# Kernel optimization log

Measured on AMD Instinct MI355X. Metric: run time of the kernel, lower is better.

The kernel has to match this reference:

```python
import jax, jax.numpy as jnp
import numpy as np

B, S, HID = 2, 2048, 2560
NH, NKV, HD = 8, 4, 256
Q_SIZE, KV_SIZE = NH * HD, NKV * HD
SCALE = 256.0 ** -0.5
SLIDING_WINDOW = 1024 - 1  # config.sliding_window - 1
ROPE_BASE = 10000.0
EPS = 1e-6


def rmsnorm(x, w, eps=EPS):
    xf = x.astype(jnp.float32)
    out = xf * jax.lax.rsqrt(jnp.mean(xf * xf, axis=-1, keepdims=True) + eps)
    return (out * (1.0 + w.astype(jnp.float32))).astype(x.dtype)


def apply_rope(x, positions):
    # x: [B,S,H,D], neox style (rotate halves)
    d = x.shape[-1]
    inv_freq = 1.0 / (ROPE_BASE ** (jnp.arange(0, d, 2, dtype=jnp.float32) / d))
    freqs = positions.astype(jnp.float32)[..., None] * inv_freq  # [B,S,d/2]
    cos = jnp.cos(freqs)[:, :, None, :]
    sin = jnp.sin(freqs)[:, :, None, :]
    x1, x2 = x[..., : d // 2], x[..., d // 2:]
    return jnp.concatenate([x1 * cos - x2 * sin, x2 * cos + x1 * sin], axis=-1).astype(x.dtype)


def setup_inputs() -> dict:
    key = jax.random.key(0)
    ks = jax.random.split(key, 4)
    positions = jnp.broadcast_to(jnp.arange(S, dtype=jnp.int32)[None, :], (B, S))
    hidden_states = jax.random.normal(ks[0], (B, S, HID), dtype=jnp.float32)
    attention_mask = jnp.ones((B, S), dtype=jnp.int32)
    Wqkv = jax.random.normal(ks[1], (HID, Q_SIZE + 2 * KV_SIZE), dtype=jnp.float32) * (HID ** -0.5)
    Wo = jax.random.normal(ks[2], (Q_SIZE, HID), dtype=jnp.float32) * (Q_SIZE ** -0.5)
    q_norm_w = jnp.zeros((HD,), dtype=jnp.float32)
    k_norm_w = jnp.zeros((HD,), dtype=jnp.float32)
    return {"positions": positions, "hidden_states": hidden_states,
            "attention_mask": attention_mask, "Wqkv": Wqkv, "Wo": Wo,
            "q_norm_w": q_norm_w, "k_norm_w": k_norm_w}


def reference(positions, hidden_states, attention_mask, Wqkv, Wo, q_norm_w, k_norm_w):
    b, s, _ = hidden_states.shape
    qkv = hidden_states @ Wqkv
    q, k, v = jnp.split(qkv, [Q_SIZE, Q_SIZE + KV_SIZE], axis=-1)
    q = q.reshape(b, s, NH, HD)
    k = k.reshape(b, s, NKV, HD)
    v = v.reshape(b, s, NKV, HD)
    q = rmsnorm(q, q_norm_w)
    k = rmsnorm(k, k_norm_w)
    q = apply_rope(q, positions)
    k = apply_rope(k, positions)

    # additive mask, replicating source exactly
    idx = jnp.arange(s)
    causal = idx[None, :] > idx[:, None]             # triu(diag=1)
    too_far = (idx[None, :] - idx[:, None]) > SLIDING_WINDOW
    base_mask = causal | too_far                      # [S,S]
    key_pad = attention_mask.astype(bool) == False    # [B,S]
    masked = base_mask[None, None, :, :] | key_pad[:, None, None, :]  # [B,1,S,S]
    add_mask = jnp.where(masked, -jnp.inf, 0.0).astype(jnp.float32)

    # GQA: group queries over kv heads
    g = NH // NKV
    qg = q.reshape(b, s, NKV, g, HD)
    scores = jnp.einsum('bsmgd,btmd->bmgst', qg, k) * SCALE  # [B,NKV,g,S,S]
    scores = scores + add_mask[:, :, None, :, :]
    probs = jax.nn.softmax(scores, axis=-1)
    out = jnp.einsum('bmgst,btmd->bsmgd', probs, v)           # [B,S,NKV,g,HD]
    out = out.reshape(b, s, NH * HD)
    return out @ Wo
```

## Files before the change

kernel.cpp:

```cpp
#include <hip/hip_runtime.h>
#include <stdint.h>

#define S_LEN 2048
#define BATCH 2
#define HIDDEN 2560
#define NH 8
#define NKV 4
#define HD 256
#define QSZ (NH*HD)
#define NQKV 4096
#define MROWS (BATCH*S_LEN)
#define SCALE_ATT 0.0625f

using bf16x8 = __attribute__((__ext_vector_type__(8))) __bf16;
using f32x4  = __attribute__((__ext_vector_type__(4))) float;
using s16x8  = __attribute__((__ext_vector_type__(8))) short;

union B8u { s16x8 s; bf16x8 b; };
union I4B8 { int4 i; bf16x8 b; };

__device__ __forceinline__ unsigned short f2bf(float x){
  unsigned u = __float_as_uint(x);
  u += 0x7fffu + ((u >> 16) & 1u);
  return (unsigned short)(u >> 16);
}
__device__ __forceinline__ bf16x8 ld_bf8(const unsigned short* p){
  B8u u; u.s = *reinterpret_cast<const s16x8*>(p); return u.b;
}
__device__ __forceinline__ f32x4 mfma16(bf16x8 a, bf16x8 b, f32x4 c){
  return __builtin_amdgcn_mfma_f32_16x16x32_bf16(a, b, c, 0, 0, 0);
}
__device__ __forceinline__ void gload16(const void* g, void* l){
  __builtin_amdgcn_global_load_lds((const __attribute__((address_space(1))) void*)g,
                                   (__attribute__((address_space(3))) void*)l,
                                   16, 0, 0);
}
__device__ __forceinline__ int cvtpk(float lo, float hi){
  int r;
  asm("v_cvt_pk_bf16_f32 %0, %1, %2" : "=v"(r) : "v"(lo), "v"(hi));
  return r;
}

__global__ __launch_bounds__(256) void cast_bf16_kernel(
    const float* __restrict__ in, unsigned short* __restrict__ out, int n)
{
  int i = (blockIdx.x * 256 + threadIdx.x) * 4;
  if (i < n){
    float4 v = *reinterpret_cast<const float4*>(in + i);
    ushort4 o;
    o.x = f2bf(v.x); o.y = f2bf(v.y); o.z = f2bf(v.z); o.w = f2bf(v.w);
    *reinterpret_cast<ushort4*>(out + i) = o;
  }
}

__global__ __launch_bounds__(256) void tcast_kernel(
    const float* __restrict__ in, unsigned short* __restrict__ out, int R, int C)
{
  __shared__ float t[32][33];
  int c0 = blockIdx.x * 32, r0 = blockIdx.y * 32;
  int tx = threadIdx.x & 31, ty = threadIdx.x >> 5;
#pragma unroll
  for (int ii = 0; ii < 4; ii++)
    t[ty + ii*8][tx] = in[(size_t)(r0 + ty + ii*8) * C + c0 + tx];
  __syncthreads();
#pragma unroll
  for (int ii = 0; ii < 4; ii++)
    out[(size_t)(c0 + ty + ii*8) * R + r0 + tx] = f2bf(t[tx][ty + ii*8]);
}

__global__ __launch_bounds__(256) void ropetab_kernel(
    const int* __restrict__ positions, float* __restrict__ ct, float* __restrict__ st)
{
  const int cix = blockIdx.x;
  const int b   = blockIdx.y;
  const float kln = -9.210340371976184f / 128.0f;
  const float inv = expf((float)cix * kln);
  float* cp = ct + ((size_t)b * 128 + cix) * 2048;
  float* sp = st + ((size_t)b * 128 + cix) * 2048;
  for (int s = threadIdx.x; s < S_LEN; s += 256){
    float fpos = (float)positions[b * S_LEN + s];
    float sv, cv;
    sincosf(fpos * inv, &sv, &cv);
    cp[s] = cv;
    sp[s] = sv;
  }
}

__global__ __launch_bounds__(512, 2) void gemm_qkv_kernel(
    const unsigned short* __restrict__ A,
    const unsigned short* __restrict__ BT,
    const float* __restrict__ qw, const float* __restrict__ kw,
    const float* __restrict__ ct, const float* __restrict__ st,
    unsigned short* __restrict__ qB,
    unsigned short* __restrict__ kB,
    unsigned short* __restrict__ vT)
{
  __shared__ unsigned short Ab[2][256 * 64];
  __shared__ unsigned short Bb[2][256 * 64];

  const int K = HIDDEN;
  const int nbn = 16;
  const int tid  = threadIdx.x;
  const int lane = tid & 63;
  const int wid  = tid >> 6;
  const int wm = wid >> 2, wn = wid & 3;
  const int lq = lane & 15, lk = lane >> 4;

  const int cpx = gridDim.x >> 3;
  const int wg  = (blockIdx.x & 7) * cpx + (blockIdx.x >> 3);
  const int bm = wg / nbn, bn = wg % nbn;

  const int l8 = lane >> 3;
  const int sl = ((lane & 7) ^ l8) * 8;
  const unsigned short* agS = A  + (size_t)(bm*256 + wid*16 + l8) * K + sl;
  const unsigned short* bgS = BT + (size_t)(bn*256 + wid*16 + l8) * K + sl;

  f32x4 acc[4][4][2] = {};
  bf16x8 a[4][2], b[2][2];

#define STA(c, h, tt) do {                                                    \
    unsigned short* d = &Ab[c][(h)*8192 + wid*1024];                          \
    const unsigned short* s = agS + (size_t)(h)*128*K + (size_t)(tt)*64;      \
    gload16(s, d); gload16(s + 8*(size_t)K, d + 512);                         \
  } while (0)
#define STB(c, h, tt) do {                                                    \
    unsigned short* d = &Bb[c][(h)*8192 + wid*1024];                          \
    const unsigned short* s = bgS + (size_t)(h)*128*K + (size_t)(tt)*64;      \
    gload16(s, d); gload16(s + 8*(size_t)K, d + 512);                         \
  } while (0)
#define LDA(qa) do {                                                          \
    _Pragma("unroll") for (int m = 0; m < 4; m++)                             \
    _Pragma("unroll") for (int kk = 0; kk < 2; kk++)                          \
      a[m][kk] = ld_bf8(&Ab[cur][((qa)*128 + wm*64 + m*16 + lq)*64            \
                                 + (((kk*4 + lk) ^ (lq & 7)) << 3)]);         \
  } while (0)
#define LDB(qb) do {                                                          \
    _Pragma("unroll") for (int n = 0; n < 2; n++)                             \
    _Pragma("unroll") for (int kk = 0; kk < 2; kk++)                          \
      b[n][kk] = ld_bf8(&Bb[cur][((qb)*128 + wn*32 + n*16 + lq)*64            \
                                 + (((kk*4 + lk) ^ (lq & 7)) << 3)]);         \
  } while (0)
#define MM(qi) do {                                                           \
    __builtin_amdgcn_s_setprio(1);                                            \
    _Pragma("unroll") for (int m = 0; m < 4; m++)                             \
    _Pragma("unroll") for (int n = 0; n < 2; n++)                             \
    _Pragma("unroll") for (int kk = 0; kk < 2; kk++)                          \
      acc[qi][m][n] = mfma16(a[m][kk], b[n][kk], acc[qi][m][n]);              \
    __builtin_amdgcn_s_setprio(0);                                            \
  } while (0)
#define BARR __builtin_amdgcn_s_barrier()
#define VM(n) asm volatile("s_waitcnt vmcnt(" #n ")" ::: "memory")

  STA(0, 0, 0); STB(0, 0, 0); STB(0, 1, 0); STA(0, 1, 0);
  VM(4); BARR;

  const int NT = K >> 6;
  for (int t = 0; t < NT - 1; ++t){
    const int cur = t & 1, nxt = cur ^ 1;
    LDA(0); LDB(0); STA(nxt, 0, t+1);
    BARR; MM(0); VM(4); BARR;
    LDB(1);         STB(nxt, 0, t+1);
    BARR; MM(1); VM(4); BARR;
    LDA(1);         STB(nxt, 1, t+1);
    BARR; MM(2);        BARR;
    LDB(0);         STA(nxt, 1, t+1);
    BARR; MM(3); VM(4); BARR;
  }
  {
    const int cur = (NT - 1) & 1;
    LDA(0); LDB(0); BARR; MM(0); VM(2); BARR;
    LDB(1);         BARR; MM(1); VM(0); BARR;
    LDA(1);         BARR; MM(2);        BARR;
    LDB(0);         BARR; MM(3);        BARR;
  }
#undef STA
#undef STB
#undef LDA
#undef LDB
#undef MM
#undef BARR
#undef VM

  __syncthreads();
  const int b_  = bm >> 3;
  const int sb0 = (bm & 7) * 256;

  if (bn >= 12){
    const int mhv = bn - 12;
#pragma unroll
    for (int qi = 0; qi < 4; qi++){
      const int qa = qi >> 1, qb = (qi ^ (qi >> 1)) & 1;
#pragma unroll
      for (int m = 0; m < 4; m++){
        const int s0 = sb0 + qa*128 + wm*64 + m*16 + lk*4;
#pragma unroll
        for (int n = 0; n < 2; n++){
          const int d = qb*128 + wn*32 + n*16 + lq;
          ushort4 o;
          o.x = f2bf(acc[qi][m][n][0]);
          o.y = f2bf(acc[qi][m][n][1]);
          o.z = f2bf(acc[qi][m][n][2]);
          o.w = f2bf(acc[qi][m][n][3]);
          *reinterpret_cast<ushort4*>(
              vT + ((size_t)((b_*NKV + mhv)*HD + d))*S_LEN + s0) = o;
        }
      }
    }
  } else {
    float* red = (float*)Ab;
    float part[2][4][4];
#pragma unroll
    for (int qa = 0; qa < 2; qa++){
      const int qiA = qa ? 3 : 0, qiB = qa ? 2 : 1;
#pragma unroll
      for (int m = 0; m < 4; m++)
#pragma unroll
      for (int i = 0; i < 4; i++){
        float s = 0.f;
#pragma unroll
        for (int n = 0; n < 2; n++)
          s += acc[qiA][m][n][i]*acc[qiA][m][n][i]
             + acc[qiB][m][n][i]*acc[qiB][m][n][i];
        s += __shfl_xor(s, 1, 64);
        s += __shfl_xor(s, 2, 64);
        s += __shfl_xor(s, 4, 64);
        s += __shfl_xor(s, 8, 64);
        part[qa][m][i] = s;
      }
    }
    if (lq == 0){
#pragma unroll
      for (int qa = 0; qa < 2; qa++)
#pragma unroll
      for (int m = 0; m < 4; m++)
#pragma unroll
      for (int i = 0; i < 4; i++)
        red[wn*256 + qa*128 + wm*64 + m*16 + lk*4 + i] = part[qa][m][i];
    }
    __syncthreads();
    float rsv[2][4][4];
#pragma unroll
    for (int qa = 0; qa < 2; qa++)
#pragma unroll
    for (int m = 0; m < 4; m++)
#pragma unroll
    for (int i = 0; i < 4; i++){
      const int row = qa*128 + wm*64 + m*16 + lk*4 + i;
      float tt = red[row] + red[256 + row] + red[512 + row] + red[768 + row];
      rsv[qa][m][i] = rsqrtf(tt * (1.0f/256.0f) + 1e-6f);
    }
    const float* wv = (bn < 8) ? qw : kw;
    unsigned short* dstB = (bn < 8)
      ? qB + ((size_t)(b_*NH  + bn      ) * S_LEN) * HD
      : kB + ((size_t)(b_*NKV + (bn - 8)) * S_LEN) * HD;
    const float* ctb = ct + (size_t)b_ * 128 * 2048;
    const float* stb = st + (size_t)b_ * 128 * 2048;
#pragma unroll
    for (int qa = 0; qa < 2; qa++){
      const int qiA = qa ? 3 : 0, qiB = qa ? 2 : 1;
#pragma unroll
      for (int m = 0; m < 4; m++){
        const int s0 = sb0 + qa*128 + wm*64 + m*16 + lk*4;
#pragma unroll
        for (int n = 0; n < 2; n++){
          const int c0 = wn*32 + n*16 + lq;
          const float w0 = 1.0f + wv[c0];
          const float w1 = 1.0f + wv[c0 + 128];
          const float4 c4 = *reinterpret_cast<const float4*>(ctb + (size_t)c0*2048 + s0);
          const float4 s4 = *reinterpret_cast<const float4*>(stb + (size_t)c0*2048 + s0);
#pragma unroll
          for (int i = 0; i < 4; i++){
            const float rs_ = rsv[qa][m][i];
            const float y0 = acc[qiA][m][n][i] * rs_ * w0;
            const float y1 = acc[qiB][m][n][i] * rs_ * w1;
            const float cc = (&c4.x)[i], ss = (&s4.x)[i];
            unsigned short* p = dstB + (size_t)(s0 + i) * HD;
            p[c0]       = f2bf(y0 * cc - y1 * ss);
            p[c0 + 128] = f2bf(y1 * cc + y0 * ss);
          }
        }
      }
    }
  }
}

__global__ __launch_bounds__(512, 2) void gemm256_kernel(
    const unsigned short* __restrict__ A,
    const unsigned short* __restrict__ BT,
    float* __restrict__ C,
    int N, int K, int nbn)
{
  __shared__ unsigned short Ab[2][256 * 64];
  __shared__ unsigned short Bb[2][256 * 64];

  const int tid  = threadIdx.x;
  const int lane = tid & 63;
  const int wid  = tid >> 6;
  const int wm = wid >> 2, wn = wid & 3;
  const int lq = lane & 15, lk = lane >> 4;

  const int cpx = gridDim.x >> 3;
  const int wg  = (blockIdx.x & 7) * cpx + (blockIdx.x >> 3);
  const int bm = wg / nbn, bn = wg % nbn;

  const int l8 = lane >> 3;
  const int sl = ((lane & 7) ^ l8) * 8;
  const unsigned short* agS = A  + (size_t)(bm*256 + wid*16 + l8) * K + sl;
  const unsigned short* bgS = BT + (size_t)(bn*256 + wid*16 + l8) * K + sl;

  f32x4 acc[4][4][2] = {};
  bf16x8 a[4][2], b[2][2];

#define STA(c, h, tt) do {                                                    \
    unsigned short* d = &Ab[c][(h)*8192 + wid*1024];                          \
    const unsigned short* s = agS + (size_t)(h)*128*K + (size_t)(tt)*64;      \
    gload16(s, d); gload16(s + 8*(size_t)K, d + 512);                         \
  } while (0)
#define STB(c, h, tt) do {                                                    \
    unsigned short* d = &Bb[c][(h)*8192 + wid*1024];                          \
    const unsigned short* s = bgS + (size_t)(h)*128*K + (size_t)(tt)*64;      \
    gload16(s, d); gload16(s + 8*(size_t)K, d + 512);                         \
  } while (0)
#define LDA(qa) do {                                                          \
    _Pragma("unroll") for (int m = 0; m < 4; m++)                             \
    _Pragma("unroll") for (int kk = 0; kk < 2; kk++)                          \
      a[m][kk] = ld_bf8(&Ab[cur][((qa)*128 + wm*64 + m*16 + lq)*64            \
                                 + (((kk*4 + lk) ^ (lq & 7)) << 3)]);         \
  } while (0)
#define LDB(qb) do {                                                          \
    _Pragma("unroll") for (int n = 0; n < 2; n++)                             \
    _Pragma("unroll") for (int kk = 0; kk < 2; kk++)                          \
      b[n][kk] = ld_bf8(&Bb[cur][((qb)*128 + wn*32 + n*16 + lq)*64            \
                                 + (((kk*4 + lk) ^ (lq & 7)) << 3)]);         \
  } while (0)
#define MM(qi) do {                                                           \
    __builtin_amdgcn_s_setprio(1);                                            \
    _Pragma("unroll") for (int m = 0; m < 4; m++)                             \
    _Pragma("unroll") for (int n = 0; n < 2; n++)                             \
    _Pragma("unroll") for (int kk = 0; kk < 2; kk++)                          \
      acc[qi][m][n] = mfma16(a[m][kk], b[n][kk], acc[qi][m][n]);              \
    __builtin_amdgcn_s_setprio(0);                                            \
  } while (0)
#define BARR __builtin_amdgcn_s_barrier()
#define VM(n) asm volatile("s_waitcnt vmcnt(" #n ")" ::: "memory")

  STA(0, 0, 0); STB(0, 0, 0); STB(0, 1, 0); STA(0, 1, 0);
  VM(4); BARR;

  const int NT = K >> 6;
  for (int t = 0; t < NT - 1; ++t){
    const int cur = t & 1, nxt = cur ^ 1;
    LDA(0); LDB(0); STA(nxt, 0, t+1);
    BARR; MM(0); VM(4); BARR;
    LDB(1);         STB(nxt, 0, t+1);
    BARR; MM(1); VM(4); BARR;
    LDA(1);         STB(nxt, 1, t+1);
    BARR; MM(2);        BARR;
    LDB(0);         STA(nxt, 1, t+1);
    BARR; MM(3); VM(4); BARR;
  }
  {
    const int cur = (NT - 1) & 1;
    LDA(0); LDB(0); BARR; MM(0); VM(2); BARR;
    LDB(1);         BARR; MM(1); VM(0); BARR;
    LDA(1);         BARR; MM(2);        BARR;
    LDB(0);         BARR; MM(3);        BARR;
  }
#undef STA
#undef STB
#undef LDA
#undef LDB
#undef MM
#undef BARR
#undef VM

#pragma unroll
  for (int qi = 0; qi < 4; qi++){
    const int qa = qi >> 1;
    const int qb = (qi ^ (qi >> 1)) & 1;
    const int r0 = bm*256 + qa*128 + wm*64;
    const int c0 = bn*256 + qb*128 + wn*32;
#pragma unroll
    for (int m = 0; m < 4; m++)
#pragma unroll
      for (int n = 0; n < 2; n++)
#pragma unroll
        for (int i = 0; i < 4; i++)
          C[(size_t)(r0 + m*16 + lk*4 + i) * N + (c0 + n*16 + lq)] = acc[qi][m][n][i];
  }
}

__global__ void maskbits_kernel(const int* __restrict__ amask, unsigned* __restrict__ bm,
                                int* __restrict__ ctr)
{
  int t = threadIdx.x;
  int b = t >> 6, tile = t & 63;
  unsigned m = 0;
  for (int j = 0; j < 32; j++)
    m |= (amask[b * S_LEN + tile * 32 + j] != 0 ? 1u : 0u) << j;
  bm[t] = m;
  if (t < 8) ctr[t] = 0;
}

__global__ __launch_bounds__(256) void attn_kernel(
    const unsigned short* __restrict__ qB,
    const unsigned short* __restrict__ kB,
    const unsigned short* __restrict__ vT,
    const unsigned* __restrict__ bmG,
    unsigned short* __restrict__ attnO,
    int* __restrict__ ctr)
{
  __shared__ unsigned short Kb[4][32 * 256];
  __shared__ unsigned short Vb[4][256 * 32];
  __shared__ unsigned bm_lds[64];
  __shared__ int s_idx;

  const int tid  = threadIdx.x;
  const int lane = tid & 63, wid = tid >> 6;
  const int c  = blockIdx.x & 7;
  const int mh = c & 3, b = c >> 2;
  const int h  = mh * 2 + (wid >> 1);
  const int lq = lane & 15, lk = lane >> 4;

  if (tid < 64) bm_lds[tid] = bmG[(b << 6) + tid];

  const unsigned short* kbase = kB + (size_t)(b * NKV + mh) * S_LEN * HD;
  const unsigned short* vbase = vT + (size_t)(b * NKV + mh) * HD * S_LEN;
  const int krow0 = wid * 2 + (lane >> 5);
  const int kgsrc = (lane & 31) ^ (krow0 & 7);
  const unsigned short* kg0 = kbase + (size_t)krow0 * HD + kgsrc * 8;
  const int vd0 = wid * 16 + (lane >> 2);
  const int vgsrc = (lane & 3) ^ ((lane >> 3) & 3);
  const unsigned short* vg0 = vbase + (size_t)vd0 * S_LEN + vgsrc * 8;

#define STAGE_K(buf, ktv)                                                      \
  do {                                                                         \
    _Pragma("unroll")                                                          \
    for (int r = 0; r < 4; r++)                                                \
      gload16(kg0 + (size_t)(ktv) * HD + r * (8 * HD),                         \
              &Kb[buf][wid * 512 + r * 2048]);                                 \
  } while (0)
#define STAGE_V(buf, ktv)                                                      \
  do {                                                                         \
    _Pragma("unroll")                                                          \
    for (int r = 0; r < 4; r++)                                                \
      gload16(vg0 + (ktv) + (size_t)r * (64 * S_LEN),                          \
              &Vb[buf][wid * 512 + r * 2048]);                                 \
  } while (0)

  for (;;){
    if (tid == 0) s_idx = atomicAdd(&ctr[c], 1);
    __syncthreads();
    const int idx = s_idx;
    __syncthreads();
    if (idx >= 64) break;
    const int qt = 63 - idx;

    const int q0 = qt * 32 + (wid & 1) * 16;
    const int q  = q0 + lq;

    const unsigned short* qbase = qB + ((size_t)(b * NH + h) * S_LEN + q0 + lq) * HD + lk * 8;
    bf16x8 aq[8];
#pragma unroll
    for (int ks = 0; ks < 8; ks++) aq[ks] = ld_bf8(qbase + ks * 32);
    asm volatile("s_waitcnt vmcnt(0)" ::: "memory");

    float mi = -__builtin_inff(), li = 0.f;
    f32x4 oacc[16] = {};

    STAGE_K(0, 0); STAGE_V(0, 0);
    if (qt >= 1){ STAGE_K(1, 32); STAGE_V(1, 32); }
    if (qt >= 2){ STAGE_K(2, 64); STAGE_V(2, 64); }
    if (qt >= 3){ STAGE_K(3, 96); STAGE_V(3, 96); }

    const int npairs = (qt >> 1) + 1;
    for (int p = 0; p < npairs; ++p){
      const int ktA = p * 64;
      const int ktB = ktA + 32;
      const bool hasB = (2*p + 1 <= qt);
      const int bufA = (2*p) & 3, bufB = (2*p + 1) & 3;

      const int ahead = qt - 2*p - 1;
      if (ahead >= 2)      asm volatile("s_waitcnt vmcnt(16)" ::: "memory");
      else if (ahead == 1) asm volatile("s_waitcnt vmcnt(8)"  ::: "memory");
      else                 asm volatile("s_waitcnt vmcnt(0)"  ::: "memory");
      __syncthreads();

      f32x4 sA0 = {0.f,0.f,0.f,0.f}, sA1 = {0.f,0.f,0.f,0.f};
      f32x4 sB0 = {0.f,0.f,0.f,0.f}, sB1 = {0.f,0.f,0.f,0.f};
      if (hasB){
#pragma unroll
        for (int ks = 0; ks < 8; ks++){
          const int slot = (((ks * 4 + lk) ^ (lq & 7)) << 3);
          bf16x8 kA0 = ld_bf8(&Kb[bufA][lq * 256 + slot]);
          bf16x8 kA1 = ld_bf8(&Kb[bufA][(16 + lq) * 256 + slot]);
          bf16x8 kB0 = ld_bf8(&Kb[bufB][lq * 256 + slot]);
          bf16x8 kB1 = ld_bf8(&Kb[bufB][(16 + lq) * 256 + slot]);
          sA0 = mfma16(kA0, aq[ks], sA0);
          sA1 = mfma16(kA1, aq[ks], sA1);
          sB0 = mfma16(kB0, aq[ks], sB0);
          sB1 = mfma16(kB1, aq[ks], sB1);
        }
      } else {
#pragma unroll
        for (int ks = 0; ks < 8; ks++){
          const int slot = (((ks * 4 + lk) ^ (lq & 7)) << 3);
          bf16x8 kA0 = ld_bf8(&Kb[bufA][lq * 256 + slot]);
          bf16x8 kA1 = ld_bf8(&Kb[bufA][(16 + lq) * 256 + slot]);
          sA0 = mfma16(kA0, aq[ks], sA0);
          sA1 = mfma16(kA1, aq[ks], sA1);
        }
      }

      const unsigned mA = bm_lds[ktA >> 5];
      const unsigned mB = bm_lds[(ktB >> 5) & 63];
      const int koff = lk * 4;
      float vA0[4], vA1[4], vB0[4], vB1[4];
#pragma unroll
      for (int j2 = 0; j2 < 4; j2++){
        const bool a0 = (ktA + koff + j2 <= q)      && ((mA >> (koff + j2)) & 1u);
        const bool a1 = (ktA + 16 + koff + j2 <= q) && ((mA >> (16 + koff + j2)) & 1u);
        vA0[j2] = a0 ? sA0[j2] * SCALE_ATT : -__builtin_inff();
        vA1[j2] = a1 ? sA1[j2] * SCALE_ATT : -__builtin_inff();
      }
      if (hasB){
#pragma unroll
        for (int j2 = 0; j2 < 4; j2++){
          const bool b0 = (ktB + koff + j2 <= q)      && ((mB >> (koff + j2)) & 1u);
          const bool b1 = (ktB + 16 + koff + j2 <= q) && ((mB >> (16 + koff + j2)) & 1u);
          vB0[j2] = b0 ? sB0[j2] * SCALE_ATT : -__builtin_inff();
          vB1[j2] = b1 ? sB1[j2] * SCALE_ATT : -__builtin_inff();
        }
      } else {
#pragma unroll
        for (int j2 = 0; j2 < 4; j2++){ vB0[j2] = -__builtin_inff(); vB1[j2] = -__builtin_inff(); }
      }
      float tm = fmaxf(fmaxf(fmaxf(vA0[0], vA0[1]), fmaxf(vA0[2], vA0[3])),
                       fmaxf(fmaxf(vA1[0], vA1[1]), fmaxf(vA1[2], vA1[3])));
      if (hasB){
        float tb = fmaxf(fmaxf(fmaxf(vB0[0], vB0[1]), fmaxf(vB0[2], vB0[3])),
                         fmaxf(fmaxf(vB1[0], vB1[1]), fmaxf(vB1[2], vB1[3])));
        tm = fmaxf(tm, tb);
      }
      tm = fmaxf(tm, __shfl_xor(tm, 16, 64));
      tm = fmaxf(tm, __shfl_xor(tm, 32, 64));

      float pA0[4], pA1[4], pB0[4], pB1[4];
      if (__all(tm <= mi + 8.0f)){
        const float mns = fmaxf(mi, -1e30f);
#pragma unroll
        for (int j2 = 0; j2 < 4; j2++){
          pA0[j2] = __expf(vA0[j2] - mns); pA1[j2] = __expf(vA1[j2] - mns);
          pB0[j2] = __expf(vB0[j2] - mns); pB1[j2] = __expf(vB1[j2] - mns);
        }
        float rs = (pA0[0]+pA0[1])+(pA0[2]+pA0[3])+(pA1[0]+pA1[1])+(pA1[2]+pA1[3])
                 + (pB0[0]+pB0[1])+(pB0[2]+pB0[3])+(pB1[0]+pB1[1])+(pB1[2]+pB1[3]);
        rs += __shfl_xor(rs, 16, 64);
        rs += __shfl_xor(rs, 32, 64);
        li += rs;
      } else {
        const float mn  = fmaxf(mi, tm);
        const float mns = fmaxf(mn, -1e30f);
#pragma unroll
        for (int j2 = 0; j2 < 4; j2++){
          pA0[j2] = __expf(vA0[j2] - mns); pA1[j2] = __expf(vA1[j2] - mns);
          pB0[j2] = __expf(vB0[j2] - mns); pB1[j2] = __expf(vB1[j2] - mns);
        }
        const float a_ = __expf(mi - mns);
        float rs = (pA0[0]+pA0[1])+(pA0[2]+pA0[3])+(pA1[0]+pA1[1])+(pA1[2]+pA1[3])
                 + (pB0[0]+pB0[1])+(pB0[2]+pB0[3])+(pB1[0]+pB1[1])+(pB1[2]+pB1[3]);
        rs += __shfl_xor(rs, 16, 64);
        rs += __shfl_xor(rs, 32, 64);
        li = li * a_ + rs;
        mi = mn;
        float av[4];
#pragma unroll
        for (int i = 0; i < 4; i++)
          av[i] = __shfl(a_, (lane & 48) | (lk * 4 + i), 64);
#pragma unroll
        for (int db = 0; db < 16; db++){
          f32x4 o = oacc[db];
#pragma unroll
          for (int i = 0; i < 4; i++) o[i] *= av[i];
          oacc[db] = o;
        }
      }

      const int sA_ = (((lk & 1) * 2) << 4) | lq;
      const int sB_ = sA_ + 16;
      const bool hi = (lk >= 2);
      I4B8 pauA, pauB;
      {
        const int w0 = cvtpk(pA0[0], pA0[1]), w1 = cvtpk(pA0[2], pA0[3]);
        const int w2 = cvtpk(pA1[0], pA1[1]), w3 = cvtpk(pA1[2], pA1[3]);
        const int a0 = __shfl(w0, sA_, 64), a1 = __shfl(w1, sA_, 64);
        const int b0 = __shfl(w0, sB_, 64), b1 = __shfl(w1, sB_, 64);
        const int c0w = __shfl(w2, sA_, 64), c1w = __shfl(w3, sA_, 64);
        const int d0w = __shfl(w2, sB_, 64), d1w = __shfl(w3, sB_, 64);
        pauA.i.x = hi ? c0w : a0;
        pauA.i.y = hi ? c1w : a1;
        pauA.i.z = hi ? d0w : b0;
        pauA.i.w = hi ? d1w : b1;
      }
      if (hasB){
        const int w0 = cvtpk(pB0[0], pB0[1]), w1 = cvtpk(pB0[2], pB0[3]);
        const int w2 = cvtpk(pB1[0], pB1[1]), w3 = cvtpk(pB1[2], pB1[3]);
        const int a0 = __shfl(w0, sA_, 64), a1 = __shfl(w1, sA_, 64);
        const int b0 = __shfl(w0, sB_, 64), b1 = __shfl(w1, sB_, 64);
        const int c0w = __shfl(w2, sA_, 64), c1w = __shfl(w3, sA_, 64);
        const int d0w = __shfl(w2, sB_, 64), d1w = __shfl(w3, sB_, 64);
        pauB.i.x = hi ? c0w : a0;
        pauB.i.y = hi ? c1w : a1;
        pauB.i.z = hi ? d0w : b0;
        pauB.i.w = hi ? d1w : b1;
      }

      const int vslot = (lk ^ ((lq >> 1) & 3)) << 3;
      if (hasB){
#pragma unroll
        for (int db = 0; db < 16; db++){
          bf16x8 vfA = ld_bf8(&Vb[bufA][(db * 16 + lq) * 32 + vslot]);
          bf16x8 vfB = ld_bf8(&Vb[bufB][(db * 16 + lq) * 32 + vslot]);
          f32x4 o = mfma16(pauA.b, vfA, oacc[db]);
          oacc[db] = mfma16(pauB.b, vfB, o);
        }
      } else {
#pragma unroll
        for (int db = 0; db < 16; db++){
          bf16x8 vfA = ld_bf8(&Vb[bufA][(db * 16 + lq) * 32 + vslot]);
          oacc[db] = mfma16(pauA.b, vfA, oacc[db]);
        }
      }

      __syncthreads();
      if (2*p + 4 <= qt){ STAGE_K(bufA, ktA + 128); STAGE_V(bufA, ktA + 128); }
      if (2*p + 5 <= qt){ STAGE_K(bufB, ktB + 128); STAGE_V(bufB, ktB + 128); }
    }

#pragma unroll
    for (int i = 0; i < 4; i++){
      const float lf = __shfl(li, (lane & 48) | (lk * 4 + i), 64);
      const float inv = 1.0f / lf;
      unsigned short* orow = attnO + (size_t)(b * S_LEN + q0 + lk*4 + i) * QSZ + h * HD + lq;
#pragma unroll
      for (int db = 0; db < 16; db++)
        orow[db * 16] = f2bf(oacc[db][i] * inv);
    }
  }
#undef STAGE_K
#undef STAGE_V
}

extern "C" void kernel_launch(void* const* d_in, const int* in_sizes, int n_in,
                              void* d_out, int out_size, void* d_ws, size_t ws_size,
                              hipStream_t stream)
{
  const int*   positions = (const int*)  d_in[0];
  const float* hidden    = (const float*)d_in[1];
  const int*   amask     = (const int*)  d_in[2];
  const float* Wqkv      = (const float*)d_in[3];
  const float* Wo        = (const float*)d_in[4];
  const float* qw        = (const float*)d_in[5];
  const float* kw        = (const float*)d_in[6];
  float* out = (float*)d_out;

  char* ws = (char*)d_ws;
  unsigned short* hB    = (unsigned short*)(ws);
  unsigned short* attnO = (unsigned short*)(ws);
  unsigned short* WqT   = (unsigned short*)(ws + 20971520);
  unsigned short* WoT   = (unsigned short*)(ws + 41943040);
  float*          ct    = (float*)        (ws + 52428800);
  float*          st    = (float*)        (ws + 56623104);
  unsigned short* qb    = (unsigned short*)(ws + 119537664);
  unsigned short* kb    = (unsigned short*)(ws + 136314880);
  unsigned short* vt    = (unsigned short*)(ws + 144703488);
  unsigned*       bm    = (unsigned*)     (ws + 153092096);
  int*            ctr   = (int*)          (ws + 153092608);

  cast_bf16_kernel<<<dim3(MROWS * HIDDEN / 1024), 256, 0, stream>>>(hidden, hB, MROWS * HIDDEN);
  tcast_kernel<<<dim3(NQKV / 32, HIDDEN / 32), 256, 0, stream>>>(Wqkv, WqT, HIDDEN, NQKV);
  tcast_kernel<<<dim3(HIDDEN / 32, QSZ / 32), 256, 0, stream>>>(Wo, WoT, QSZ, HIDDEN);
  maskbits_kernel<<<dim3(1), 128, 0, stream>>>(amask, bm, ctr);
  ropetab_kernel<<<dim3(128, BATCH), 256, 0, stream>>>(positions, ct, st);

  gemm_qkv_kernel<<<dim3((MROWS/256) * (NQKV/256)), 512, 0, stream>>>(
      hB, WqT, qw, kw, ct, st, qb, kb, vt);

  attn_kernel<<<dim3(256), 256, 0, stream>>>(qb, kb, vt, bm, attnO, ctr);

  gemm256_kernel<<<dim3((MROWS/256) * (HIDDEN/256)), 512, 0, stream>>>(
      attnO, WoT, out, HIDDEN, QSZ, HIDDEN/256);
}
```

Before: 317.7 us.

## Process two 16-row query blocks per wave to reuse K/V fragments

Each wave now handles 32 query rows (two 16-row sub-tiles) per work item, so every K and V fragment read from LDS feeds two MFMAs. Work items drop from 64 to 32 per (batch, kv-head) group. The K/V staging goes from four buffers with paired tiles to two buffers with one tile per step. This halves LDS traffic per unit of compute and frees shared memory. In exchange it doubles the accumulator and Q registers, which may lower occupancy, and coarser query tiles add causal-masked waste and worse load balance near the diagonal.

```diff
diff --git a/kernel.cpp b/kernel.cpp
--- a/kernel.cpp
+++ b/kernel.cpp
@@ -410,8 +410,8 @@
     unsigned short* __restrict__ attnO,
     int* __restrict__ ctr)
 {
-  __shared__ unsigned short Kb[4][32 * 256];
-  __shared__ unsigned short Vb[4][256 * 32];
+  __shared__ unsigned short Kb[2][32 * 256];
+  __shared__ unsigned short Vb[2][256 * 32];
   __shared__ unsigned bm_lds[64];
   __shared__ int s_idx;
 
@@ -453,143 +453,131 @@
     __syncthreads();
     const int idx = s_idx;
     __syncthreads();
-    if (idx >= 64) break;
-    const int qt = 63 - idx;
-
-    const int q0 = qt * 32 + (wid & 1) * 16;
-    const int q  = q0 + lq;
-
-    const unsigned short* qbase = qB + ((size_t)(b * NH + h) * S_LEN + q0 + lq) * HD + lk * 8;
-    bf16x8 aq[8];
-#pragma unroll
-    for (int ks = 0; ks < 8; ks++) aq[ks] = ld_bf8(qbase + ks * 32);
+    if (idx >= 32) break;
+    const int qt = 31 - idx;
+
+    const int q0 = qt * 64 + (wid & 1) * 32;
+    const int qr0 = q0 + lq;
+    const int qr1 = q0 + 16 + lq;
+
+    const unsigned short* qbase = qB + ((size_t)(b * NH + h) * S_LEN + qr0) * HD + lk * 8;
+    bf16x8 aq0[8], aq1[8];
+#pragma unroll
+    for (int ks = 0; ks < 8; ks++){
+      aq0[ks] = ld_bf8(qbase + ks * 32);
+      aq1[ks] = ld_bf8(qbase + 16 * HD + ks * 32);
+    }
     asm volatile("s_waitcnt vmcnt(0)" ::: "memory");
 
-    float mi = -__builtin_inff(), li = 0.f;
-    f32x4 oacc[16] = {};
-
-    STAGE_K(0, 0); STAGE_V(0, 0);
-    if (qt >= 1){ STAGE_K(1, 32); STAGE_V(1, 32); }
-    if (qt >= 2){ STAGE_K(2, 64); STAGE_V(2, 64); }
-    if (qt >= 3){ STAGE_K(3, 96); STAGE_V(3, 96); }
-
-    const int npairs = (qt >> 1) + 1;
-    for (int p = 0; p < npairs; ++p){
-      const int ktA = p * 64;
-      const int ktB = ktA + 32;
-      const bool hasB = (2*p + 1 <= qt);
-      const int bufA = (2*p) & 3, bufB = (2*p + 1) & 3;
-
-      const int ahead = qt - 2*p - 1;
-      if (ahead >= 2)      asm volatile("s_waitcnt vmcnt(16)" ::: "memory");
-      else if (ahead == 1) asm volatile("s_waitcnt vmcnt(8)"  ::: "memory");
-      else                 asm volatile("s_waitcnt vmcnt(0)"  ::: "memory");
+    float mi0 = -__builtin_inff(), li0 = 0.f;
+    float mi1 = -__builtin_inff(), li1 = 0.f;
+    f32x4 oacc0[16] = {};
+    f32x4 oacc1[16] = {};
+
+    const int ktmax = qt * 64 + 32;
+
+    STAGE_K(0, 0);  STAGE_V(0, 0);
+    STAGE_K(1, 32); STAGE_V(1, 32);
+
+    int cur = 0;
+    for (int kt = 0; kt <= ktmax; kt += 32, cur ^= 1){
+      if (kt < ktmax) asm volatile("s_waitcnt vmcnt(8)" ::: "memory");
+      else            asm volatile("s_waitcnt vmcnt(0)" ::: "memory");
       __syncthreads();
 
       f32x4 sA0 = {0.f,0.f,0.f,0.f}, sA1 = {0.f,0.f,0.f,0.f};
-      f32x4 sB0 = {0.f,0.f,0.f,0.f}, sB1 = {0.f,0.f,0.f,0.f};
-      if (hasB){
-#pragma unroll
-        for (int ks = 0; ks < 8; ks++){
-          const int slot = (((ks * 4 + lk) ^ (lq & 7)) << 3);
-          bf16x8 kA0 = ld_bf8(&Kb[bufA][lq * 256 + slot]);
-          bf16x8 kA1 = ld_bf8(&Kb[bufA][(16 + lq) * 256 + slot]);
-          bf16x8 kB0 = ld_bf8(&Kb[bufB][lq * 256 + slot]);
-          bf16x8 kB1 = ld_bf8(&Kb[bufB][(16 + lq) * 256 + slot]);
-          sA0 = mfma16(kA0, aq[ks], sA0);
-          sA1 = mfma16(kA1, aq[ks], sA1);
-          sB0 = mfma16(kB0, aq[ks], sB0);
-          sB1 = mfma16(kB1, aq[ks], sB1);
+      f32x4 sC0 = {0.f,0.f,0.f,0.f}, sC1 = {0.f,0.f,0.f,0.f};
+#pragma unroll
+      for (int ks = 0; ks < 8; ks++){
+        const int slot = (((ks * 4 + lk) ^ (lq & 7)) << 3);
+        bf16x8 kf0 = ld_bf8(&Kb[cur][lq * 256 + slot]);
+        bf16x8 kf1 = ld_bf8(&Kb[cur][(16 + lq) * 256 + slot]);
+        sA0 = mfma16(kf0, aq0[ks], sA0);
+        sA1 = mfma16(kf1, aq0[ks], sA1);
+        sC0 = mfma16(kf0, aq1[ks], sC0);
+        sC1 = mfma16(kf1, aq1[ks], sC1);
+      }
+
+      const unsigned mask32 = bm_lds[kt >> 5];
+      const int koff = lk * 4;
+      float vA0[4], vA1[4], vC0[4], vC1[4];
+#pragma unroll
+      for (int j2 = 0; j2 < 4; j2++){
+        const bool m0 = ((mask32 >> (koff + j2)) & 1u);
+        const bool m1 = ((mask32 >> (16 + koff + j2)) & 1u);
+        const int k0 = kt + koff + j2, k1 = kt + 16 + koff + j2;
+        vA0[j2] = (k0 <= qr0 && m0) ? sA0[j2] * SCALE_ATT : -__builtin_inff();
+        vA1[j2] = (k1 <= qr0 && m1) ? sA1[j2] * SCALE_ATT : -__builtin_inff();
+        vC0[j2] = (k0 <= qr1 && m0) ? sC0[j2] * SCALE_ATT : -__builtin_inff();
+        vC1[j2] = (k1 <= qr1 && m1) ? sC1[j2] * SCALE_ATT : -__builtin_inff();
+      }
+      float tm0 = fmaxf(fmaxf(fmaxf(vA0[0], vA0[1]), fmaxf(vA0[2], vA0[3])),
+                        fmaxf(fmaxf(vA1[0], vA1[1]), fmaxf(vA1[2], vA1[3])));
+      float tm1 = fmaxf(fmaxf(fmaxf(vC0[0], vC0[1]), fmaxf(vC0[2], vC0[3])),
+                        fmaxf(fmaxf(vC1[0], vC1[1]), fmaxf(vC1[2], vC1[3])));
+      tm0 = fmaxf(tm0, __shfl_xor(tm0, 16, 64));
+      tm0 = fmaxf(tm0, __shfl_xor(tm0, 32, 64));
+      tm1 = fmaxf(tm1, __shfl_xor(tm1, 16, 64));
+      tm1 = fmaxf(tm1, __shfl_xor(tm1, 32, 64));
+
+      float pA0[4], pA1[4], pC0[4], pC1[4];
+      if (__all(tm0 <= mi0 + 8.0f && tm1 <= mi1 + 8.0f)){
+        const float mns0 = fmaxf(mi0, -1e30f);
+        const float mns1 = fmaxf(mi1, -1e30f);
+#pragma unroll
+        for (int j2 = 0; j2 < 4; j2++){
+          pA0[j2] = __expf(vA0[j2] - mns0); pA1[j2] = __expf(vA1[j2] - mns0);
+          pC0[j2] = __expf(vC0[j2] - mns1); pC1[j2] = __expf(vC1[j2] - mns1);
         }
+        float rs0 = (pA0[0]+pA0[1])+(pA0[2]+pA0[3])+(pA1[0]+pA1[1])+(pA1[2]+pA1[3]);
+        float rs1 = (pC0[0]+pC0[1])+(pC0[2]+pC0[3])+(pC1[0]+pC1[1])+(pC1[2]+pC1[3]);
+        rs0 += __shfl_xor(rs0, 16, 64);
+        rs0 += __shfl_xor(rs0, 32, 64);
+        rs1 += __shfl_xor(rs1, 16, 64);
+        rs1 += __shfl_xor(rs1, 32, 64);
+        li0 += rs0;
+        li1 += rs1;
       } else {
-#pragma unroll
-        for (int ks = 0; ks < 8; ks++){
-          const int slot = (((ks * 4 + lk) ^ (lq & 7)) << 3);
-          bf16x8 kA0 = ld_bf8(&Kb[bufA][lq * 256 + slot]);
-          bf16x8 kA1 = ld_bf8(&Kb[bufA][(16 + lq) * 256 + slot]);
-          sA0 = mfma16(kA0, aq[ks], sA0);
-          sA1 = mfma16(kA1, aq[ks], sA1);
+        const float mn0  = fmaxf(mi0, tm0);
+        const float mn1  = fmaxf(mi1, tm1);
+        const float mns0 = fmaxf(mn0, -1e30f);
+        const float mns1 = fmaxf(mn1, -1e30f);
+#pragma unroll
+        for (int j2 = 0; j2 < 4; j2++){
+          pA0[j2] = __expf(vA0[j2] - mns0); pA1[j2] = __expf(vA1[j2] - mns0);
+          pC0[j2] = __expf(vC0[j2] - mns1); pC1[j2] = __expf(vC1[j2] - mns1);
         }
-      }
-
-      const unsigned mA = bm_lds[ktA >> 5];
-      const unsigned mB = bm_lds[(ktB >> 5) & 63];
-      const int koff = lk * 4;
-      float vA0[4], vA1[4], vB0[4], vB1[4];
-#pragma unroll
-      for (int j2 = 0; j2 < 4; j2++){
-        const bool a0 = (ktA + koff + j2 <= q)      && ((mA >> (koff + j2)) & 1u);
-        const bool a1 = (ktA + 16 + koff + j2 <= q) && ((mA >> (16 + koff + j2)) & 1u);
-        vA0[j2] = a0 ? sA0[j2] * SCALE_ATT : -__builtin_inff();
-        vA1[j2] = a1 ? sA1[j2] * SCALE_ATT : -__builtin_inff();
-      }
-      if (hasB){
-#pragma unroll
-        for (int j2 = 0; j2 < 4; j2++){
-          const bool b0 = (ktB + koff + j2 <= q)      && ((mB >> (koff + j2)) & 1u);
-          const bool b1 = (ktB + 16 + koff + j2 <= q) && ((mB >> (16 + koff + j2)) & 1u);
-          vB0[j2] = b0 ? sB0[j2] * SCALE_ATT : -__builtin_inff();
-          vB1[j2] = b1 ? sB1[j2] * SCALE_ATT : -__builtin_inff();
+        const float a0_ = __expf(mi0 - mns0);
+        const float a1_ = __expf(mi1 - mns1);
+        float rs0 = (pA0[0]+pA0[1])+(pA0[2]+pA0[3])+(pA1[0]+pA1[1])+(pA1[2]+pA1[3]);
+        float rs1 = (pC0[0]+pC0[1])+(pC0[2]+pC0[3])+(pC1[0]+pC1[1])+(pC1[2]+pC1[3]);
+        rs0 += __shfl_xor(rs0, 16, 64);
+        rs0 += __shfl_xor(rs0, 32, 64);
+        rs1 += __shfl_xor(rs1, 16, 64);
+        rs1 += __shfl_xor(rs1, 32, 64);
+        li0 = li0 * a0_ + rs0;
+        li1 = li1 * a1_ + rs1;
+        mi0 = mn0;
+        mi1 = mn1;
+        float av0[4], av1[4];
+#pragma unroll
+        for (int i = 0; i < 4; i++){
+          av0[i] = __shfl(a0_, (lane & 48) | (lk * 4 + i), 64);
+          av1[i] = __shfl(a1_, (lane & 48) | (lk * 4 + i), 64);
         }
-      } else {
-#pragma unroll
-        for (int j2 = 0; j2 < 4; j2++){ vB0[j2] = -__builtin_inff(); vB1[j2] = -__builtin_inff(); }
-      }
-      float tm = fmaxf(fmaxf(fmaxf(vA0[0], vA0[1]), fmaxf(vA0[2], vA0[3])),
-                       fmaxf(fmaxf(vA1[0], vA1[1]), fmaxf(vA1[2], vA1[3])));
-      if (hasB){
-        float tb = fmaxf(fmaxf(fmaxf(vB0[0], vB0[1]), fmaxf(vB0[2], vB0[3])),
-                         fmaxf(fmaxf(vB1[0], vB1[1]), fmaxf(vB1[2], vB1[3])));
-        tm = fmaxf(tm, tb);
-      }
-      tm = fmaxf(tm, __shfl_xor(tm, 16, 64));
-      tm = fmaxf(tm, __shfl_xor(tm, 32, 64));
-
-      float pA0[4], pA1[4], pB0[4], pB1[4];
-      if (__all(tm <= mi + 8.0f)){
-        const float mns = fmaxf(mi, -1e30f);
-#pragma unroll
-        for (int j2 = 0; j2 < 4; j2++){
-          pA0[j2] = __expf(vA0[j2] - mns); pA1[j2] = __expf(vA1[j2] - mns);
-          pB0[j2] = __expf(vB0[j2] - mns); pB1[j2] = __expf(vB1[j2] - mns);
-        }
-        float rs = (pA0[0]+pA0[1])+(pA0[2]+pA0[3])+(pA1[0]+pA1[1])+(pA1[2]+pA1[3])
-                 + (pB0[0]+pB0[1])+(pB0[2]+pB0[3])+(pB1[0]+pB1[1])+(pB1[2]+pB1[3]);
-        rs += __shfl_xor(rs, 16, 64);
-        rs += __shfl_xor(rs, 32, 64);
-        li += rs;
-      } else {
-        const float mn  = fmaxf(mi, tm);
-        const float mns = fmaxf(mn, -1e30f);
-#pragma unroll
-        for (int j2 = 0; j2 < 4; j2++){
-          pA0[j2] = __expf(vA0[j2] - mns); pA1[j2] = __expf(vA1[j2] - mns);
-          pB0[j2] = __expf(vB0[j2] - mns); pB1[j2] = __expf(vB1[j2] - mns);
-        }
-        const float a_ = __expf(mi - mns);
-        float rs = (pA0[0]+pA0[1])+(pA0[2]+pA0[3])+(pA1[0]+pA1[1])+(pA1[2]+pA1[3])
-                 + (pB0[0]+pB0[1])+(pB0[2]+pB0[3])+(pB1[0]+pB1[1])+(pB1[2]+pB1[3]);
-        rs += __shfl_xor(rs, 16, 64);
-        rs += __shfl_xor(rs, 32, 64);
-        li = li * a_ + rs;
-        mi = mn;
-        float av[4];
-#pragma unroll
-        for (int i = 0; i < 4; i++)
-          av[i] = __shfl(a_, (lane & 48) | (lk * 4 + i), 64);
 #pragma unroll
         for (int db = 0; db < 16; db++){
-          f32x4 o = oacc[db];
-#pragma unroll
-          for (int i = 0; i < 4; i++) o[i] *= av[i];
-          oacc[db] = o;
+          f32x4 o0 = oacc0[db], o1 = oacc1[db];
+#pragma unroll
+          for (int i = 0; i < 4; i++){ o0[i] *= av0[i]; o1[i] *= av1[i]; }
+          oacc0[db] = o0; oacc1[db] = o1;
         }
       }
 
       const int sA_ = (((lk & 1) * 2) << 4) | lq;
       const int sB_ = sA_ + 16;
       const bool hi = (lk >= 2);
-      I4B8 pauA, pauB;
+      I4B8 pau0, pau1;
       {
         const int w0 = cvtpk(pA0[0], pA0[1]), w1 = cvtpk(pA0[2], pA0[3]);
         const int w2 = cvtpk(pA1[0], pA1[1]), w3 = cvtpk(pA1[2], pA1[3]);
@@ -597,54 +585,49 @@
         const int b0 = __shfl(w0, sB_, 64), b1 = __shfl(w1, sB_, 64);
         const int c0w = __shfl(w2, sA_, 64), c1w = __shfl(w3, sA_, 64);
         const int d0w = __shfl(w2, sB_, 64), d1w = __shfl(w3, sB_, 64);
-        pauA.i.x = hi ? c0w : a0;
-        pauA.i.y = hi ? c1w : a1;
-        pauA.i.z = hi ? d0w : b0;
-        pauA.i.w = hi ? d1w : b1;
-      }
-      if (hasB){
-        const int w0 = cvtpk(pB0[0], pB0[1]), w1 = cvtpk(pB0[2], pB0[3]);
-        const int w2 = cvtpk(pB1[0], pB1[1]), w3 = cvtpk(pB1[2], pB1[3]);
+        pau0.i.x = hi ? c0w : a0;
+        pau0.i.y = hi ? c1w : a1;
+        pau0.i.z = hi ? d0w : b0;
+        pau0.i.w = hi ? d1w : b1;
+      }
+      {
+        const int w0 = cvtpk(pC0[0], pC0[1]), w1 = cvtpk(pC0[2], pC0[3]);
+        const int w2 = cvtpk(pC1[0], pC1[1]), w3 = cvtpk(pC1[2], pC1[3]);
         const int a0 = __shfl(w0, sA_, 64), a1 = __shfl(w1, sA_, 64);
         const int b0 = __shfl(w0, sB_, 64), b1 = __shfl(w1, sB_, 64);
         const int c0w = __shfl(w2, sA_, 64), c1w = __shfl(w3, sA_, 64);
         const int d0w = __shfl(w2, sB_, 64), d1w = __shfl(w3, sB_, 64);
-        pauB.i.x = hi ? c0w : a0;
-        pauB.i.y = hi ? c1w : a1;
-        pauB.i.z = hi ? d0w : b0;
-        pauB.i.w = hi ? d1w : b1;
+        pau1.i.x = hi ? c0w : a0;
+        pau1.i.y = hi ? c1w : a1;
+        pau1.i.z = hi ? d0w : b0;
+        pau1.i.w = hi ? d1w : b1;
       }
 
       const int vslot = (lk ^ ((lq >> 1) & 3)) << 3;
-      if (hasB){
-#pragma unroll
-        for (int db = 0; db < 16; db++){
-          bf16x8 vfA = ld_bf8(&Vb[bufA][(db * 16 + lq) * 32 + vslot]);
-          bf16x8 vfB = ld_bf8(&Vb[bufB][(db * 16 + lq) * 32 + vslot]);
-          f32x4 o = mfma16(pauA.b, vfA, oacc[db]);
-          oacc[db] = mfma16(pauB.b, vfB, o);
-        }
-      } else {
-#pragma unroll
-        for (int db = 0; db < 16; db++){
-          bf16x8 vfA = ld_bf8(&Vb[bufA][(db * 16 + lq) * 32 + vslot]);
-          oacc[db] = mfma16(pauA.b, vfA, oacc[db]);
-        }
+#pragma unroll
+      for (int db = 0; db < 16; db++){
+        bf16x8 vf = ld_bf8(&Vb[cur][(db * 16 + lq) * 32 + vslot]);
+        oacc0[db] = mfma16(pau0.b, vf, oacc0[db]);
+        oacc1[db] = mfma16(pau1.b, vf, oacc1[db]);
       }
 
       __syncthreads();
-      if (2*p + 4 <= qt){ STAGE_K(bufA, ktA + 128); STAGE_V(bufA, ktA + 128); }
-      if (2*p + 5 <= qt){ STAGE_K(bufB, ktB + 128); STAGE_V(bufB, ktB + 128); }
+      if (kt + 64 <= ktmax){ STAGE_K(cur, kt + 64); STAGE_V(cur, kt + 64); }
     }
 
 #pragma unroll
     for (int i = 0; i < 4; i++){
-      const float lf = __shfl(li, (lane & 48) | (lk * 4 + i), 64);
-      const float inv = 1.0f / lf;
-      unsigned short* orow = attnO + (size_t)(b * S_LEN + q0 + lk*4 + i) * QSZ + h * HD + lq;
-#pragma unroll
-      for (int db = 0; db < 16; db++)
-        orow[db * 16] = f2bf(oacc[db][i] * inv);
+      const float lf0 = __shfl(li0, (lane & 48) | (lk * 4 + i), 64);
+      const float lf1 = __shfl(li1, (lane & 48) | (lk * 4 + i), 64);
+      const float inv0 = 1.0f / lf0;
+      const float inv1 = 1.0f / lf1;
+      unsigned short* orow0 = attnO + (size_t)(b * S_LEN + q0      + lk*4 + i) * QSZ + h * HD + lq;
+      unsigned short* orow1 = attnO + (size_t)(b * S_LEN + q0 + 16 + lk*4 + i) * QSZ + h * HD + lq;
+#pragma unroll
+      for (int db = 0; db < 16; db++){
+        orow0[db * 16] = f2bf(oacc0[db][i] * inv0);
+        orow1[db * 16] = f2bf(oacc1[db][i] * inv1);
+      }
     }
   }
 #undef STAGE_K
```

Measured after the change: 414.6 us. 30.5% more time.
